# Kernel tuning notes

Measured on AMD Instinct MI355X. Metric: run time of the kernel, lower is better.

The kernel has to match this reference:

```python
import jax, jax.numpy as jnp
import numpy as np

VOCAB = 32000
DIM = 512
B = 1
T = 2048
RANK = 64
TOPK = 16
SLOTS = (256, 64, 16)
INTERVALS = (1, 4, 16)
WIN = 64
PLAYERS = 2
LN_EPS = 1e-5
STD = 0.02


def setup_inputs() -> dict:
    key = jax.random.key(0)
    ks = jax.random.split(key, 12)
    return {
        "input_ids": jax.random.randint(ks[0], (B, T), 0, VOCAB),
        "E": jax.random.normal(ks[1], (VOCAB, DIM), jnp.float32) * STD,
        "Ur": jax.random.normal(ks[2], (3, DIM, RANK), jnp.float32) * STD,
        "Vr": jax.random.normal(ks[3], (3, DIM, RANK), jnp.float32) * STD,
        "m0_0": jax.random.normal(ks[4], (B, SLOTS[0], DIM), jnp.float32) * STD,
        "m0_1": jax.random.normal(ks[5], (B, SLOTS[1], DIM), jnp.float32) * STD,
        "m0_2": jax.random.normal(ks[6], (B, SLOTS[2], DIM), jnp.float32) * STD,
        "Wproj": jax.random.normal(ks[7], (DIM, DIM), jnp.float32) * STD,
        "Wq": jax.random.normal(ks[8], (PLAYERS, DIM, RANK), jnp.float32) * STD,
        "Wk": jax.random.normal(ks[9], (PLAYERS, DIM, RANK), jnp.float32) * STD,
        "ln_in_g": jnp.ones((DIM,), jnp.float32),
        "ln_in_b": jnp.zeros((DIM,), jnp.float32),
        "ln_pred_g": jnp.ones((PLAYERS, DIM), jnp.float32),
        "ln_pred_b": jnp.zeros((PLAYERS, DIM), jnp.float32),
        "ln_out_g": jnp.ones((DIM,), jnp.float32),
        "ln_out_b": jnp.zeros((DIM,), jnp.float32),
    }


def _ln(x, g, b):
    m = jnp.mean(x, axis=-1, keepdims=True)
    v = jnp.mean(jnp.square(x - m), axis=-1, keepdims=True)
    return (x - m) * jax.lax.rsqrt(v + LN_EPS) * g + b


def _memory_scan(s, Ur, Vr, m_init):
    # s: [B, N, D] aligned sequence values; m_init: tuple of [B, S_l, D]
    scale = 1.0 / jnp.sqrt(jnp.float32(RANK))
    x_seq = jnp.swapaxes(s, 0, 1)  # [N, B, D]
    ts = jnp.arange(x_seq.shape[0])
    barange = jnp.arange(s.shape[0])[:, None]

    def step(carry, xs):
        x, t = xs  # x: [B, D]
        read = x
        new_mem = []
        for l, interval in enumerate(INTERVALS):
            M = carry[l]  # [B, S_l, D]
            qr = x @ Ur[l]                                   # [B, r]
            kr = jnp.einsum('bsd,dr->bsr', M, Vr[l])         # [B, S_l, r]
            sc = jnp.einsum('br,bsr->bs', qr, kr) * scale    # low-rank bilinear route
            vals, idx = jax.lax.top_k(sc, TOPK)              # top-k slot routing
            w = jax.nn.softmax(vals, axis=-1)                # [B, K]
            sel = jnp.take_along_axis(M, idx[..., None], axis=1)  # [B, K, D]
            read = read + jnp.einsum('bk,bkd->bd', w, sel)
            gate = jnp.where(t % interval == 0, 1.0, 0.0).astype(x.dtype)
            delta = gate * w[..., None] * x[:, None, :]      # [B, K, D]
            new_mem.append(M.at[barange, idx].add(delta))    # scatter write
        return tuple(new_mem), read

    final_mem, reads = jax.lax.scan(step, m_init, (x_seq, ts))
    return final_mem, jnp.swapaxes(reads, 0, 1)  # [B, N, D]


def reference(input_ids, E, Ur, Vr, m0_0, m0_1, m0_2, Wproj, Wq, Wk,
              ln_in_g, ln_in_b, ln_pred_g, ln_pred_b, ln_out_g, ln_out_b):
    emb = E[input_ids]            # [B, T, D]
    s = emb[:, 1:, :]             # aligned_s = val[:, 1:, :]
    N = s.shape[1]
    scale = 1.0 / jnp.sqrt(jnp.float32(RANK))

    _, q = _memory_scan(s, Ur, Vr, (m0_0, m0_1, m0_2))
    h = _ln(q @ Wproj.T, ln_in_g, ln_in_b)

    offs = jnp.arange(-WIN + 1, 1)
    idx = jnp.arange(N)[:, None] + offs[None, :]   # [N, W]
    valid = idx >= 0
    idxc = jnp.clip(idx, 0, N - 1)

    for p in range(PLAYERS):
        a = jnp.einsum('bnd,dr->bnr', h, Wq[p])
        kf = jnp.einsum('bnd,dr->bnr', h, Wk[p])
        kw = kf[:, idxc]                                       # [B, N, W, r]
        vw = h[:, idxc]                                        # [B, N, W, D]
        sc = jnp.einsum('bnr,bnwr->bnw', a, kw) * scale
        # signed_abs_softmax edge compression
        logits = jnp.where(valid[None], jnp.abs(sc), -1e9)
        w = jax.nn.softmax(logits, axis=-1) * jnp.sign(sc) * valid[None]
        delta = jnp.einsum('bnw,bnwd->bnd', w, vw)
        h = _ln(h + delta, ln_pred_g[p], ln_pred_b[p])         # residual + norm

    out = _ln(h, ln_out_g, ln_out_b)
    return jnp.einsum('bnd,vd->bnv', out, E)  # tied embedding head
```

## Files before the change

### kernel.cpp

```cpp
#include <hip/hip_runtime.h>

#define N_SEQ 2047
#define DIM   512
#define RANK  64
#define VOCAB 32000
#define SCALE 0.125f
#define LN_EPS 1e-5f

typedef __attribute__((ext_vector_type(4))) float  floatx4;
typedef __attribute__((ext_vector_type(8))) __bf16 bf16x8;
typedef __attribute__((ext_vector_type(4))) unsigned short ushortx4;

__device__ __forceinline__ unsigned short f2bf(float x) {
    unsigned int u = __builtin_bit_cast(unsigned int, x);
    return (unsigned short)((u + 0x7fffu + ((u >> 16) & 1u)) >> 16);
}

__device__ __forceinline__ float wave_sum64(float x) {
    int xi;
    xi = __builtin_amdgcn_update_dpp(0, __float_as_int(x), 0x111, 0xf, 0xf, false); x += __int_as_float(xi);
    xi = __builtin_amdgcn_update_dpp(0, __float_as_int(x), 0x112, 0xf, 0xf, false); x += __int_as_float(xi);
    xi = __builtin_amdgcn_update_dpp(0, __float_as_int(x), 0x114, 0xf, 0xf, false); x += __int_as_float(xi);
    xi = __builtin_amdgcn_update_dpp(0, __float_as_int(x), 0x118, 0xf, 0xf, false); x += __int_as_float(xi);
    xi = __builtin_amdgcn_update_dpp(0, __float_as_int(x), 0x142, 0xa, 0xf, false); x += __int_as_float(xi);
    xi = __builtin_amdgcn_update_dpp(0, __float_as_int(x), 0x143, 0x8, 0xf, false); x += __int_as_float(xi);
    return __int_as_float(__builtin_amdgcn_readlane(__float_as_int(x), 63));
}

__global__ __launch_bounds__(128) void k_embed(const int* __restrict__ ids,
                                               const float* __restrict__ E,
                                               float* __restrict__ s,
                                               float* __restrict__ q) {
    int n = blockIdx.x;
    int id = ids[n + 1];
    float4 v = ((const float4*)(E + (size_t)id * DIM))[threadIdx.x];
    ((float4*)(s + (size_t)n * DIM))[threadIdx.x] = v;
    ((float4*)(q + (size_t)n * DIM))[threadIdx.x] = v;
}

__global__ __launch_bounds__(384) void k_proj(const float* __restrict__ s,
                                              const float* __restrict__ Ur,
                                              const float* __restrict__ Vr,
                                              float* __restrict__ qr,
                                              float* __restrict__ xv) {
    __shared__ float s8[8 * DIM];
    int t0 = blockIdx.x * 8;
    for (int i = threadIdx.x; i < 8 * DIM; i += 384) {
        int t = t0 + (i >> 9);
        s8[i] = (t < N_SEQ) ? s[(size_t)t * DIM + (i & 511)] : 0.f;
    }
    __syncthreads();
    int c = threadIdx.x;
    int l = (c % 192) / 64;
    int r = c & 63;
    const float* W = ((c < 192) ? Ur : Vr) + (size_t)l * DIM * RANK + r;
    float acc[8] = {};
    for (int d = 0; d < DIM; d++) {
        float w = W[(size_t)d * RANK];
        #pragma unroll
        for (int i = 0; i < 8; i++) acc[i] += s8[i * DIM + d] * w;
    }
    float* out = ((c < 192) ? qr : xv) + (size_t)l * N_SEQ * RANK;
    #pragma unroll
    for (int i = 0; i < 8; i++) {
        int t = t0 + i;
        if (t < N_SEQ) out[(size_t)t * RANK + r] = acc[i];
    }
}

__global__ __launch_bounds__(64) void k_kr0(const float* __restrict__ m0,
                                            const float* __restrict__ m1,
                                            const float* __restrict__ m2,
                                            const float* __restrict__ Vr,
                                            float* __restrict__ kr) {
    __shared__ float mrow[DIM];
    int sl = blockIdx.x;
    int lvl = (sl < 256) ? 0 : (sl < 320 ? 1 : 2);
    const float* src = (lvl == 0) ? m0 + (size_t)sl * DIM
                     : (lvl == 1) ? m1 + (size_t)(sl - 256) * DIM
                                  : m2 + (size_t)(sl - 320) * DIM;
    for (int i = threadIdx.x; i < DIM / 4; i += 64)
        ((float4*)mrow)[i] = ((const float4*)src)[i];
    __syncthreads();
    const float* W = Vr + (size_t)lvl * DIM * RANK + threadIdx.x;
    float acc = 0.f;
    for (int d = 0; d < DIM; d++) acc += mrow[d] * W[(size_t)d * RANK];
    kr[(size_t)sl * RANK + threadIdx.x] = acc;
}

#define SELECT_BODY(T, QC, QN) { \
    const int t_  = (T); \
    const int tt_ = t_ & 63; \
    const int buf_ = (t_ >> 6) & 1; \
    const int tstage_ = (t_ & ~63) + 64 + tt_; \
    if (tstage_ < N_SEQ) { \
        const float a_ = qrl[(size_t)tstage_ * RANK + lane]; \
        const float c_ = xvl[(size_t)tstage_ * RANK + lane]; \
        qs[(((buf_ ^ 1) << 6) + tt_) * 64 + lane] = a_; \
        xs[(((buf_ ^ 1) << 6) + tt_) * 64 + lane] = c_; \
    } \
    float acc_[G]; \
    _Pragma("unroll") for (int g = 0; g < G; ++g) acc_[g] = 0.f; \
    _Pragma("unroll") for (int rq = 0; rq < 16; ++rq) { \
        const float4 qf_ = QC[rq]; \
        _Pragma("unroll") for (int g = 0; g < G; ++g) { \
            acc_[g] += qf_.x * krr[g][rq * 4 + 0]; \
            acc_[g] += qf_.y * krr[g][rq * 4 + 1]; \
            acc_[g] += qf_.z * krr[g][rq * 4 + 2]; \
            acc_[g] += qf_.w * krr[g][rq * 4 + 3]; \
        } \
    } \
    { const int tn_ = t_ + 1; \
      const int off_ = ((((tn_ >> 6) & 1) << 6) + (tn_ & 63)) * 64; \
      _Pragma("unroll") for (int rq = 0; rq < 16; ++rq) QN[rq] = ((const float4*)(qs + off_))[rq]; } \
    float scf_[G]; unsigned key_[G]; \
    _Pragma("unroll") for (int g = 0; g < G; ++g) { \
        scf_[g] = acc_[g] * SCALE; \
        const unsigned b_ = __float_as_uint(scf_[g]); \
        const unsigned u_ = (b_ & 0x80000000u) ? ~b_ : (b_ | 0x80000000u); \
        key_[g] = ((g << 6) + lane < S) ? u_ : 0u; \
    } \
    unsigned thr_ = 0u; \
    _Pragma("unroll") for (int bit = 31; bit >= 0; --bit) { \
        const unsigned cand_ = thr_ | (1u << bit); \
        int cnt_ = 0; \
        _Pragma("unroll") for (int g = 0; g < G; ++g) cnt_ += (int)__popcll(__ballot(key_[g] >= cand_)); \
        if (cnt_ >= 16) thr_ = cand_; \
    } \
    unsigned long long beq_[G]; unsigned long long bsel_[G]; bool selq_[G]; \
    int cntgt_ = 0; \
    _Pragma("unroll") for (int g = 0; g < G; ++g) { \
        cntgt_ += (int)__popcll(__ballot(key_[g] > thr_)); \
        beq_[g] = __ballot(key_[g] == thr_); \
    } \
    const int needeq_ = 16 - cntgt_; \
    int eqpre_ = 0; \
    _Pragma("unroll") for (int g = 0; g < G; ++g) { \
        const bool isgt_ = key_[g] > thr_; \
        const bool iseq_ = key_[g] == thr_; \
        const int eqrank_ = eqpre_ + (int)__popcll(beq_[g] & ltmask); \
        selq_[g] = isgt_ || (iseq_ && (eqrank_ < needeq_)); \
        bsel_[g] = __ballot(selq_[g]); \
        eqpre_ += (int)__popcll(beq_[g]); \
    } \
    const unsigned tb_ = (thr_ & 0x80000000u) ? (thr_ & 0x7fffffffu) : ~thr_; \
    const float Tf_ = __uint_as_float(tb_); \
    float e_[G]; float es_ = 0.f; \
    _Pragma("unroll") for (int g = 0; g < G; ++g) { \
        e_[g] = selq_[g] ? expf(scf_[g] - Tf_) : 0.f; \
        es_ += e_[g]; \
    } \
    const float inv_ = 1.f / wave_sum64(es_); \
    int pb_ = 0; \
    _Pragma("unroll") for (int g = 0; g < G; ++g) { \
        if (selq_[g]) { \
            const int pos_ = pb_ + (int)__popcll(bsel_[g] & ltmask); \
            float2 o_; o_.x = e_[g] * inv_; o_.y = __int_as_float((g << 6) + lane); \
            selo[(size_t)t_ * 16 + pos_] = o_; \
        } \
        pb_ += (int)__popcll(bsel_[g]); \
    } \
    if ((t_ & IMASK) == 0) { \
        const float* xrow_ = xs + (((size_t)buf_ << 6) + tt_) * 64; \
        _Pragma("unroll") for (int rq = 0; rq < 16; ++rq) { \
            const float4 xf_ = ((const float4*)xrow_)[rq]; \
            _Pragma("unroll") for (int g = 0; g < G; ++g) { \
                const float wg_ = e_[g] * inv_; \
                krr[g][rq * 4 + 0] += wg_ * xf_.x; \
                krr[g][rq * 4 + 1] += wg_ * xf_.y; \
                krr[g][rq * 4 + 2] += wg_ * xf_.z; \
                krr[g][rq * 4 + 3] += wg_ * xf_.w; \
            } \
        } \
    } \
}

template<int S, int IMASK>
__device__ __forceinline__ void select_impl(float* qs, float* xs,
                                            const float* __restrict__ qrl,
                                            const float* __restrict__ xvl,
                                            const float* __restrict__ krl,
                                            float2* __restrict__ selo) {
    constexpr int G = (S + 63) / 64;
    const int lane = threadIdx.x;
    const unsigned long long ltmask = (1ULL << lane) - 1ULL;

    float krr[G][RANK];
    #pragma unroll
    for (int g = 0; g < G; ++g) {
        const int slot = (g << 6) + lane;
        if (slot < S) {
            #pragma unroll
            for (int rq = 0; rq < 16; ++rq) {
                float4 v = ((const float4*)(krl + (size_t)slot * RANK))[rq];
                krr[g][rq * 4 + 0] = v.x; krr[g][rq * 4 + 1] = v.y;
                krr[g][rq * 4 + 2] = v.z; krr[g][rq * 4 + 3] = v.w;
            }
        } else {
            #pragma unroll
            for (int r = 0; r < RANK; ++r) krr[g][r] = 0.f;
        }
    }

    for (int i = 0; i < 64; ++i) {
        qs[i * 64 + lane] = qrl[(size_t)i * RANK + lane];
        xs[i * 64 + lane] = xvl[(size_t)i * RANK + lane];
    }
    __syncthreads();

    float4 qvA[16], qvB[16];
    #pragma unroll
    for (int rq = 0; rq < 16; ++rq) qvA[rq] = ((const float4*)qs)[rq];

    int t = 0;
    for (; t + 1 < N_SEQ; t += 2) {
        SELECT_BODY(t,     qvA, qvB);
        SELECT_BODY(t + 1, qvB, qvA);
    }
    SELECT_BODY(t, qvA, qvB);
}

__global__ __launch_bounds__(64, 1) void k_select_all(const float* __restrict__ qr,
                                                      const float* __restrict__ xv,
                                                      const float* __restrict__ kr0,
                                                      float2* __restrict__ sel) {
    __shared__ float qs[2 * 64 * 64];
    __shared__ float xs[2 * 64 * 64];
    const int l = blockIdx.x;
    if (l == 0)
        select_impl<256, 0>(qs, xs, qr, xv, kr0, sel);
    else if (l == 1)
        select_impl<64, 3>(qs, xs, qr + (size_t)N_SEQ * RANK, xv + (size_t)N_SEQ * RANK,
                           kr0 + 256 * RANK, sel + (size_t)N_SEQ * 16);
    else
        select_impl<16, 15>(qs, xs, qr + (size_t)2 * N_SEQ * RANK, xv + (size_t)2 * N_SEQ * RANK,
                            kr0 + 320 * RANK, sel + (size_t)2 * N_SEQ * 16);
}

template<int S, int IMASK>
__device__ __forceinline__ void apply_impl(float* Ml,
                                           const float* __restrict__ sA,
                                           const float2* __restrict__ selo,
                                           const float* __restrict__ Msrc,
                                           float* __restrict__ q, int chunk) {
    const int lane = threadIdx.x;
    const int c0 = chunk * 64;
    for (int sl = 0; sl < S; ++sl)
        Ml[sl * 64 + lane] = Msrc[(size_t)sl * DIM + c0 + lane];
    __syncthreads();

    float4 svc[8];
    #pragma unroll
    for (int k = 0; k < 8; ++k) svc[k] = ((const float4*)selo)[k];
    float scc = sA[c0 + lane];

    for (int t = 0; t < N_SEQ; ++t) {
        float4 svn[8]; float scn;
        const int tn = (t + 1 < N_SEQ) ? t + 1 : t;
        #pragma unroll
        for (int k = 0; k < 8; ++k) svn[k] = ((const float4*)(selo + (size_t)tn * 16))[k];
        scn = sA[(size_t)tn * DIM + c0 + lane];

        const bool gate = (t & IMASK) == 0;
        float acc = 0.f;
        #pragma unroll
        for (int k = 0; k < 8; ++k) {
            const float w0 = svc[k].x; const int i0 = __float_as_int(svc[k].y);
            const float w1 = svc[k].z; const int i1 = __float_as_int(svc[k].w);
            const float m0v = Ml[i0 * 64 + lane];
            const float m1v = Ml[i1 * 64 + lane];
            acc += w0 * m0v;
            acc += w1 * m1v;
            if (gate) {
                Ml[i0 * 64 + lane] = m0v + w0 * scc;
                Ml[i1 * 64 + lane] = m1v + w1 * scc;
            }
        }
        atomicAdd(&q[(size_t)t * DIM + c0 + lane], acc);
        #pragma unroll
        for (int k = 0; k < 8; ++k) svc[k] = svn[k];
        scc = scn;
    }
}

__global__ __launch_bounds__(64) void k_apply_all(const float* __restrict__ s,
                                                  const float2* __restrict__ sel,
                                                  const float* __restrict__ m0,
                                                  const float* __restrict__ m1,
                                                  const float* __restrict__ m2,
                                                  float* __restrict__ q) {
    __shared__ float Ml[256 * 64];
    const int b = blockIdx.x;
    if (b < 8)
        apply_impl<256, 0>(Ml, s, sel, m0, q, b);
    else if (b < 16)
        apply_impl<64, 3>(Ml, s, sel + (size_t)N_SEQ * 16, m1, q, b - 8);
    else
        apply_impl<16, 15>(Ml, s, sel + (size_t)2 * N_SEQ * 16, m2, q, b - 16);
}

__global__ __launch_bounds__(256) void k_wproj_ln(const float* __restrict__ q,
                                                  const float* __restrict__ Wp,
                                                  const float* __restrict__ g,
                                                  const float* __restrict__ b,
                                                  float* __restrict__ h) {
    __shared__ float q8[8 * DIM];
    __shared__ float hp[8 * DIM];
    int t0 = blockIdx.x * 8;
    for (int i = threadIdx.x; i < 8 * DIM; i += 256) {
        int t = t0 + (i >> 9);
        q8[i] = (t < N_SEQ) ? q[(size_t)t * DIM + (i & 511)] : 0.f;
    }
    __syncthreads();
    int c0 = threadIdx.x * 2;
    float acc0[8] = {}, acc1[8] = {};
    const float* w0 = Wp + (size_t)c0 * DIM;
    const float* w1 = w0 + DIM;
    for (int d = 0; d < DIM; d++) {
        float a0 = w0[d], a1 = w1[d];
        #pragma unroll
        for (int i = 0; i < 8; i++) {
            float qv = q8[i * DIM + d];
            acc0[i] += qv * a0;
            acc1[i] += qv * a1;
        }
    }
    #pragma unroll
    for (int i = 0; i < 8; i++) {
        hp[i * DIM + c0]     = acc0[i];
        hp[i * DIM + c0 + 1] = acc1[i];
    }
    __syncthreads();
    int rowi = threadIdx.x >> 5;
    int l32  = threadIdx.x & 31;
    int t = t0 + rowi;
    if (t < N_SEQ) {
        float sum = 0.f, sq = 0.f;
        #pragma unroll
        for (int u = 0; u < 16; u++) {
            float x = hp[rowi * DIM + l32 + u * 32];
            sum += x; sq += x * x;
        }
        #pragma unroll
        for (int off = 16; off >= 1; off >>= 1) {
            sum += __shfl_xor(sum, off, 32);
            sq  += __shfl_xor(sq,  off, 32);
        }
        float mean = sum * (1.f / DIM);
        float var  = sq * (1.f / DIM) - mean * mean;
        float inv  = rsqrtf(var + LN_EPS);
        #pragma unroll
        for (int u = 0; u < 16; u++) {
            int d = l32 + u * 32;
            float x = hp[rowi * DIM + d];
            h[(size_t)t * DIM + d] = (x - mean) * inv * g[d] + b[d];
        }
    }
}

__global__ __launch_bounds__(128) void k_qk(const float* __restrict__ h,
                                            const float* __restrict__ Wq,
                                            const float* __restrict__ Wk,
                                            float* __restrict__ a,
                                            float* __restrict__ kf) {
    __shared__ float h8[8 * DIM];
    int t0 = blockIdx.x * 8;
    for (int i = threadIdx.x; i < 8 * DIM; i += 128) {
        int t = t0 + (i >> 9);
        h8[i] = (t < N_SEQ) ? h[(size_t)t * DIM + (i & 511)] : 0.f;
    }
    __syncthreads();
    int c = threadIdx.x;
    int r = c & 63;
    const float* W = ((c < 64) ? Wq : Wk) + r;
    float acc[8] = {};
    for (int d = 0; d < DIM; d++) {
        float w = W[(size_t)d * RANK];
        #pragma unroll
        for (int i = 0; i < 8; i++) acc[i] += h8[i * DIM + d] * w;
    }
    float* out = (c < 64) ? a : kf;
    #pragma unroll
    for (int i = 0; i < 8; i++) {
        int t = t0 + i;
        if (t < N_SEQ) out[(size_t)t * RANK + r] = acc[i];
    }
}

__global__ __launch_bounds__(64) void k_attn(const float* __restrict__ hin,
                                             const float* __restrict__ a,
                                             const float* __restrict__ kf,
                                             const float* __restrict__ g,
                                             const float* __restrict__ b,
                                             float* __restrict__ hout) {
    __shared__ float a_s[64];
    __shared__ float w_s[64];
    int t = blockIdx.x;
    int lane = threadIdx.x;
    a_s[lane] = a[(size_t)t * RANK + lane];
    __syncthreads();
    int src  = t - 63 + lane;
    int srcc = src < 0 ? 0 : src;
    const float* kr_ = kf + (size_t)srcc * RANK;
    float sc = 0.f;
    #pragma unroll 8
    for (int r = 0; r < RANK; r++) sc += a_s[r] * kr_[r];
    sc *= SCALE;
    float logit = (src >= 0) ? fabsf(sc) : -1e9f;
    float m = logit;
    #pragma unroll
    for (int off = 32; off >= 1; off >>= 1) m = fmaxf(m, __shfl_xor(m, off, 64));
    float e = expf(logit - m);
    float sum = e;
    #pragma unroll
    for (int off = 32; off >= 1; off >>= 1) sum += __shfl_xor(sum, off, 64);
    float sgn = (sc > 0.f) ? 1.f : ((sc < 0.f) ? -1.f : 0.f);
    float w = (src >= 0) ? (e / sum) * sgn : 0.f;
    w_s[lane] = w;
    __syncthreads();
    float acc[8] = {};
    int basej = t - 63;
    for (int j = 0; j < 64; j++) {
        float wj = w_s[j];
        int sj = basej + j; sj = sj < 0 ? 0 : sj;
        const float* hr = hin + (size_t)sj * DIM + lane;
        #pragma unroll
        for (int u = 0; u < 8; u++) acc[u] += wj * hr[u * 64];
    }
    const float* hrow = hin + (size_t)t * DIM + lane;
    float x[8]; float sum2 = 0.f, sq = 0.f;
    #pragma unroll
    for (int u = 0; u < 8; u++) {
        x[u] = hrow[u * 64] + acc[u];
        sum2 += x[u]; sq += x[u] * x[u];
    }
    #pragma unroll
    for (int off = 32; off >= 1; off >>= 1) {
        sum2 += __shfl_xor(sum2, off, 64);
        sq   += __shfl_xor(sq,   off, 64);
    }
    float mean = sum2 * (1.f / DIM);
    float var  = sq * (1.f / DIM) - mean * mean;
    float inv  = rsqrtf(var + LN_EPS);
    #pragma unroll
    for (int u = 0; u < 8; u++) {
        int d = lane + u * 64;
        hout[(size_t)t * DIM + d] = (x[u] - mean) * inv * g[d] + b[d];
    }
}

__global__ __launch_bounds__(64) void k_ln_out(const float* __restrict__ hin,
                                               const float* __restrict__ g,
                                               const float* __restrict__ b,
                                               float* __restrict__ hP) {
    int t = blockIdx.x;
    int lane = threadIdx.x;
    if (t >= N_SEQ) {
        #pragma unroll
        for (int u = 0; u < 8; u++) hP[(size_t)t * DIM + lane + u * 64] = 0.f;
        return;
    }
    const float* hrow = hin + (size_t)t * DIM + lane;
    float x[8]; float sum = 0.f, sq = 0.f;
    #pragma unroll
    for (int u = 0; u < 8; u++) {
        x[u] = hrow[u * 64];
        sum += x[u]; sq += x[u] * x[u];
    }
    #pragma unroll
    for (int off = 32; off >= 1; off >>= 1) {
        sum += __shfl_xor(sum, off, 64);
        sq  += __shfl_xor(sq,  off, 64);
    }
    float mean = sum * (1.f / DIM);
    float var  = sq * (1.f / DIM) - mean * mean;
    float inv  = rsqrtf(var + LN_EPS);
    #pragma unroll
    for (int u = 0; u < 8; u++) {
        int d = lane + u * 64;
        hP[(size_t)t * DIM + d] = (x[u] - mean) * inv * g[d] + b[d];
    }
}

__global__ __launch_bounds__(256) void k_gemm(const float* __restrict__ A,
                                              const float* __restrict__ E,
                                              float* __restrict__ C) {
    __shared__ unsigned short As[128 * 64];
    __shared__ unsigned short Bs[128 * 64];
    int bm = blockIdx.y, bn = blockIdx.x;
    int tid = threadIdx.x;
    int lane = tid & 63, wave = tid >> 6;
    int wm = (wave >> 1) << 6, wn = (wave & 1) << 6;
    floatx4 acc[4][4] = {};
    for (int k0 = 0; k0 < DIM; k0 += 64) {
        #pragma unroll
        for (int ch = 0; ch < 8; ch++) {
            int f4 = ch * 256 + tid;
            int el = f4 * 4;
            int row = el >> 6;
            int kk = el & 63;
            int csw = (kk >> 3) ^ (row & 7);
            int dst = row * 64 + csw * 8 + (kk & 7);
            float4 av = *(const float4*)(A + (size_t)(bm * 128 + row) * DIM + k0 + kk);
            ushortx4 ua = { f2bf(av.x), f2bf(av.y), f2bf(av.z), f2bf(av.w) };
            *(ushortx4*)&As[dst] = ua;
            float4 bv = *(const float4*)(E + (size_t)(bn * 128 + row) * DIM + k0 + kk);
            ushortx4 ub = { f2bf(bv.x), f2bf(bv.y), f2bf(bv.z), f2bf(bv.w) };
            *(ushortx4*)&Bs[dst] = ub;
        }
        __syncthreads();
        int mr = lane & 15, qd = lane >> 4;
        #pragma unroll
        for (int kh = 0; kh < 2; kh++) {
            bf16x8 af[4], bfr[4];
            #pragma unroll
            for (int i = 0; i < 4; i++) {
                int row = wm + i * 16 + mr;
                int c = kh * 4 + qd;
                af[i] = *(const bf16x8*)&As[row * 64 + ((c ^ (row & 7)) << 3)];
            }
            #pragma unroll
            for (int j = 0; j < 4; j++) {
                int row = wn + j * 16 + mr;
                int c = kh * 4 + qd;
                bfr[j] = *(const bf16x8*)&Bs[row * 64 + ((c ^ (row & 7)) << 3)];
            }
            #pragma unroll
            for (int i = 0; i < 4; i++)
                #pragma unroll
                for (int j = 0; j < 4; j++)
                    acc[i][j] = __builtin_amdgcn_mfma_f32_16x16x32_bf16(af[i], bfr[j], acc[i][j], 0, 0, 0);
        }
        __syncthreads();
    }
    int lr = lane >> 4, lc = lane & 15;
    #pragma unroll
    for (int i = 0; i < 4; i++)
        #pragma unroll
        for (int j = 0; j < 4; j++)
            #pragma unroll
            for (int reg = 0; reg < 4; reg++) {
                int gr = bm * 128 + wm + i * 16 + lr * 4 + reg;
                int gc = bn * 128 + wn + j * 16 + lc;
                if (gr < N_SEQ) C[(size_t)gr * VOCAB + gc] = acc[i][j][reg];
            }
}

extern "C" void kernel_launch(void* const* d_in, const int* in_sizes, int n_in,
                              void* d_out, int out_size, void* d_ws, size_t ws_size,
                              hipStream_t stream) {
    (void)in_sizes; (void)n_in; (void)out_size; (void)ws_size;
    const int*   ids  = (const int*)d_in[0];
    const float* E    = (const float*)d_in[1];
    const float* Ur   = (const float*)d_in[2];
    const float* Vr   = (const float*)d_in[3];
    const float* m0   = (const float*)d_in[4];
    const float* m1   = (const float*)d_in[5];
    const float* m2   = (const float*)d_in[6];
    const float* Wp   = (const float*)d_in[7];
    const float* Wq   = (const float*)d_in[8];
    const float* Wk   = (const float*)d_in[9];
    const float* lig  = (const float*)d_in[10];
    const float* lib  = (const float*)d_in[11];
    const float* lpg  = (const float*)d_in[12];
    const float* lpb  = (const float*)d_in[13];
    const float* log_ = (const float*)d_in[14];
    const float* lob  = (const float*)d_in[15];
    float* out = (float*)d_out;

    float* ws = (float*)d_ws;
    size_t off = 0;
    auto alloc = [&](size_t n) { float* p = ws + off; off += (n + 255) & ~(size_t)255; return p; };
    float* s   = alloc((size_t)N_SEQ * DIM);
    float* q   = alloc((size_t)N_SEQ * DIM);
    float* qr  = alloc((size_t)3 * N_SEQ * RANK);
    float* xv  = alloc((size_t)3 * N_SEQ * RANK);
    float* kr  = alloc((size_t)336 * RANK);
    float* sel = alloc((size_t)3 * N_SEQ * 16 * 2);
    float* hA  = alloc((size_t)N_SEQ * DIM);
    float* hB  = alloc((size_t)N_SEQ * DIM);
    float* ab  = alloc((size_t)N_SEQ * RANK);
    float* kfb = alloc((size_t)N_SEQ * RANK);
    float* hP  = alloc((size_t)2048 * DIM);

    k_embed     <<<N_SEQ, 128, 0, stream>>>(ids, E, s, q);
    k_proj      <<<256, 384, 0, stream>>>(s, Ur, Vr, qr, xv);
    k_kr0       <<<336, 64, 0, stream>>>(m0, m1, m2, Vr, kr);
    k_select_all<<<3, 64, 0, stream>>>(qr, xv, kr, (float2*)sel);
    k_apply_all <<<24, 64, 0, stream>>>(s, (const float2*)sel, m0, m1, m2, q);
    k_wproj_ln  <<<256, 256, 0, stream>>>(q, Wp, lig, lib, hA);
    k_qk        <<<256, 128, 0, stream>>>(hA, Wq, Wk, ab, kfb);
    k_attn      <<<N_SEQ, 64, 0, stream>>>(hA, ab, kfb, lpg, lpb, hB);
    k_qk        <<<256, 128, 0, stream>>>(hB, Wq + DIM * RANK, Wk + DIM * RANK, ab, kfb);
    k_attn      <<<N_SEQ, 64, 0, stream>>>(hB, ab, kfb, lpg + DIM, lpb + DIM, hA);
    k_ln_out    <<<2048, 64, 0, stream>>>(hA, log_, lob, hP);
    dim3 gg(VOCAB / 128, 2048 / 128);
    k_gemm      <<<gg, 256, 0, stream>>>(hP, E, out);
}
```

Measured before the change: 10.69 ms.

## Split sequential top-k select into a selector wave and score-computing worker waves

The serial memory-routing select kernel moves from one 64-thread wave per level to 320 threads. Wave 0 performs the top-k threshold search, now resolving two bits per step, and writes the selected weights to shared memory. The other waves each own one slot's key vector, apply the previous step's rank-1 update and compute the next step's score one step ahead. A diagonal correction term is added so the lookahead score matches the updated key. This shortens the per-token critical path, at the cost of two block barriers per timestep and extra shared-memory traffic.

New measurement: 9.122 ms. 1.17x faster.

```diff
diff --git a/kernel.cpp b/kernel.cpp
--- a/kernel.cpp
+++ b/kernel.cpp
@@ -88,152 +88,204 @@
     kr[(size_t)sl * RANK + threadIdx.x] = acc;
 }
 
-#define SELECT_BODY(T, QC, QN) { \
-    const int t_  = (T); \
-    const int tt_ = t_ & 63; \
-    const int buf_ = (t_ >> 6) & 1; \
-    const int tstage_ = (t_ & ~63) + 64 + tt_; \
-    if (tstage_ < N_SEQ) { \
-        const float a_ = qrl[(size_t)tstage_ * RANK + lane]; \
-        const float c_ = xvl[(size_t)tstage_ * RANK + lane]; \
-        qs[(((buf_ ^ 1) << 6) + tt_) * 64 + lane] = a_; \
-        xs[(((buf_ ^ 1) << 6) + tt_) * 64 + lane] = c_; \
-    } \
-    float acc_[G]; \
-    _Pragma("unroll") for (int g = 0; g < G; ++g) acc_[g] = 0.f; \
-    _Pragma("unroll") for (int rq = 0; rq < 16; ++rq) { \
-        const float4 qf_ = QC[rq]; \
-        _Pragma("unroll") for (int g = 0; g < G; ++g) { \
-            acc_[g] += qf_.x * krr[g][rq * 4 + 0]; \
-            acc_[g] += qf_.y * krr[g][rq * 4 + 1]; \
-            acc_[g] += qf_.z * krr[g][rq * 4 + 2]; \
-            acc_[g] += qf_.w * krr[g][rq * 4 + 3]; \
-        } \
-    } \
-    { const int tn_ = t_ + 1; \
-      const int off_ = ((((tn_ >> 6) & 1) << 6) + (tn_ & 63)) * 64; \
-      _Pragma("unroll") for (int rq = 0; rq < 16; ++rq) QN[rq] = ((const float4*)(qs + off_))[rq]; } \
-    float scf_[G]; unsigned key_[G]; \
-    _Pragma("unroll") for (int g = 0; g < G; ++g) { \
-        scf_[g] = acc_[g] * SCALE; \
-        const unsigned b_ = __float_as_uint(scf_[g]); \
-        const unsigned u_ = (b_ & 0x80000000u) ? ~b_ : (b_ | 0x80000000u); \
-        key_[g] = ((g << 6) + lane < S) ? u_ : 0u; \
-    } \
-    unsigned thr_ = 0u; \
-    _Pragma("unroll") for (int bit = 31; bit >= 0; --bit) { \
-        const unsigned cand_ = thr_ | (1u << bit); \
-        int cnt_ = 0; \
-        _Pragma("unroll") for (int g = 0; g < G; ++g) cnt_ += (int)__popcll(__ballot(key_[g] >= cand_)); \
-        if (cnt_ >= 16) thr_ = cand_; \
-    } \
-    unsigned long long beq_[G]; unsigned long long bsel_[G]; bool selq_[G]; \
-    int cntgt_ = 0; \
-    _Pragma("unroll") for (int g = 0; g < G; ++g) { \
-        cntgt_ += (int)__popcll(__ballot(key_[g] > thr_)); \
-        beq_[g] = __ballot(key_[g] == thr_); \
-    } \
-    const int needeq_ = 16 - cntgt_; \
-    int eqpre_ = 0; \
-    _Pragma("unroll") for (int g = 0; g < G; ++g) { \
-        const bool isgt_ = key_[g] > thr_; \
-        const bool iseq_ = key_[g] == thr_; \
-        const int eqrank_ = eqpre_ + (int)__popcll(beq_[g] & ltmask); \
-        selq_[g] = isgt_ || (iseq_ && (eqrank_ < needeq_)); \
-        bsel_[g] = __ballot(selq_[g]); \
-        eqpre_ += (int)__popcll(beq_[g]); \
-    } \
-    const unsigned tb_ = (thr_ & 0x80000000u) ? (thr_ & 0x7fffffffu) : ~thr_; \
-    const float Tf_ = __uint_as_float(tb_); \
-    float e_[G]; float es_ = 0.f; \
-    _Pragma("unroll") for (int g = 0; g < G; ++g) { \
-        e_[g] = selq_[g] ? expf(scf_[g] - Tf_) : 0.f; \
-        es_ += e_[g]; \
-    } \
-    const float inv_ = 1.f / wave_sum64(es_); \
-    int pb_ = 0; \
-    _Pragma("unroll") for (int g = 0; g < G; ++g) { \
-        if (selq_[g]) { \
-            const int pos_ = pb_ + (int)__popcll(bsel_[g] & ltmask); \
-            float2 o_; o_.x = e_[g] * inv_; o_.y = __int_as_float((g << 6) + lane); \
-            selo[(size_t)t_ * 16 + pos_] = o_; \
-        } \
-        pb_ += (int)__popcll(bsel_[g]); \
-    } \
-    if ((t_ & IMASK) == 0) { \
-        const float* xrow_ = xs + (((size_t)buf_ << 6) + tt_) * 64; \
-        _Pragma("unroll") for (int rq = 0; rq < 16; ++rq) { \
-            const float4 xf_ = ((const float4*)xrow_)[rq]; \
-            _Pragma("unroll") for (int g = 0; g < G; ++g) { \
-                const float wg_ = e_[g] * inv_; \
-                krr[g][rq * 4 + 0] += wg_ * xf_.x; \
-                krr[g][rq * 4 + 1] += wg_ * xf_.y; \
-                krr[g][rq * 4 + 2] += wg_ * xf_.z; \
-                krr[g][rq * 4 + 3] += wg_ * xf_.w; \
-            } \
-        } \
-    } \
-}
-
 template<int S, int IMASK>
-__device__ __forceinline__ void select_impl(float* qs, float* xs,
+__device__ __forceinline__ void select_impl(float (*qs)[32][64], float (*xs)[32][64],
+                                            float* scs, float* wsel_s, int* isel_s,
                                             const float* __restrict__ qrl,
                                             const float* __restrict__ xvl,
                                             const float* __restrict__ krl,
                                             float2* __restrict__ selo) {
     constexpr int G = (S + 63) / 64;
-    const int lane = threadIdx.x;
+    const int tid  = threadIdx.x;
+    const int wave = tid >> 6;
+    const int lane = tid & 63;
     const unsigned long long ltmask = (1ULL << lane) - 1ULL;
 
-    float krr[G][RANK];
-    #pragma unroll
-    for (int g = 0; g < G; ++g) {
-        const int slot = (g << 6) + lane;
-        if (slot < S) {
-            #pragma unroll
-            for (int rq = 0; rq < 16; ++rq) {
-                float4 v = ((const float4*)(krl + (size_t)slot * RANK))[rq];
-                krr[g][rq * 4 + 0] = v.x; krr[g][rq * 4 + 1] = v.y;
-                krr[g][rq * 4 + 2] = v.z; krr[g][rq * 4 + 3] = v.w;
+    for (int row = wave; row < 32; row += 5) {
+        qs[0][row][lane] = qrl[(size_t)row * RANK + lane];
+        xs[0][row][lane] = xvl[(size_t)row * RANK + lane];
+    }
+    if (tid < 256) scs[tid] = -3.0e38f;
+
+    const int  slot     = (wave >= 1) ? (((wave - 1) << 6) + lane) : -1;
+    const bool isWorker = (wave >= 1) && (slot < S);
+
+    float krr[RANK];
+    if (isWorker) {
+        #pragma unroll
+        for (int i = 0; i < 16; ++i)
+            ((floatx4*)krr)[i] = ((const floatx4*)(krl + (size_t)slot * RANK))[i];
+    } else {
+        #pragma unroll
+        for (int r = 0; r < RANK; ++r) krr[r] = 0.f;
+    }
+
+    float qstage = 0.f, xstage = 0.f;
+    if (wave == 1) qstage = qrl[(size_t)32 * RANK + lane];
+    if (wave == 2) xstage = xvl[(size_t)32 * RANK + lane];
+
+    __syncthreads();
+
+    if (isWorker) {
+        float acc = 0.f;
+        #pragma unroll
+        for (int i = 0; i < 16; ++i) {
+            float4 qf = ((const float4*)qs[0][0])[i];
+            acc += qf.x * krr[i*4+0] + qf.y * krr[i*4+1] + qf.z * krr[i*4+2] + qf.w * krr[i*4+3];
+        }
+        scs[slot] = acc * SCALE;
+    }
+    float wprev = 0.f;
+    __syncthreads();
+
+    for (int t = 0; t < N_SEQ; ++t) {
+        const int gate = ((t & IMASK) == 0);
+        float sc_raw = 0.f, dgl = 0.f;
+
+        if (wave == 0) {
+            float scf[G]; unsigned key[G];
+            #pragma unroll
+            for (int g = 0; g < G; ++g) {
+                float v = scs[(g << 6) + lane];
+                scf[g] = v;
+                unsigned bb = __float_as_uint(v);
+                key[g] = (bb & 0x80000000u) ? ~bb : (bb | 0x80000000u);
+            }
+            unsigned thr = 0u;
+            #pragma unroll
+            for (int bit = 30; bit >= 0; bit -= 2) {
+                const unsigned cLo = thr | (1u << bit);
+                const unsigned cHi = thr | (2u << bit);
+                const unsigned cBo = thr | (3u << bit);
+                int nLo = 0, nHi = 0, nBo = 0;
+                #pragma unroll
+                for (int g = 0; g < G; ++g) {
+                    nLo += (int)__popcll(__ballot(key[g] >= cLo));
+                    nHi += (int)__popcll(__ballot(key[g] >= cHi));
+                    nBo += (int)__popcll(__ballot(key[g] >= cBo));
+                }
+                if (nHi >= 16)      thr = (nBo >= 16) ? cBo : cHi;
+                else if (nLo >= 16) thr = cLo;
+            }
+            unsigned long long beq[G], bsel[G]; bool selq[G];
+            int cntgt = 0;
+            #pragma unroll
+            for (int g = 0; g < G; ++g) {
+                cntgt += (int)__popcll(__ballot(key[g] > thr));
+                beq[g] = __ballot(key[g] == thr);
+            }
+            const int needeq = 16 - cntgt;
+            int eqpre = 0;
+            #pragma unroll
+            for (int g = 0; g < G; ++g) {
+                const bool isgt = key[g] > thr;
+                const bool iseq = key[g] == thr;
+                const int eqrank = eqpre + (int)__popcll(beq[g] & ltmask);
+                selq[g] = isgt || (iseq && (eqrank < needeq));
+                bsel[g] = __ballot(selq[g]);
+                eqpre += (int)__popcll(beq[g]);
+            }
+            const unsigned tb = (thr & 0x80000000u) ? (thr & 0x7fffffffu) : ~thr;
+            const float Tf = __uint_as_float(tb);
+            float e[G]; float es = 0.f;
+            #pragma unroll
+            for (int g = 0; g < G; ++g) {
+                e[g] = selq[g] ? expf(scf[g] - Tf) : 0.f;
+                es += e[g];
+            }
+            const float inv = 1.f / wave_sum64(es);
+            int pb = 0;
+            #pragma unroll
+            for (int g = 0; g < G; ++g) {
+                if (selq[g]) {
+                    const int pos = pb + (int)__popcll(bsel[g] & ltmask);
+                    const float w = e[g] * inv;
+                    const int sl = (g << 6) + lane;
+                    float2 o; o.x = w; o.y = __int_as_float(sl);
+                    selo[(size_t)t * 16 + pos] = o;
+                    wsel_s[pos] = w;
+                    isel_s[pos] = sl;
+                }
+                pb += (int)__popcll(bsel[g]);
             }
         } else {
-            #pragma unroll
-            for (int r = 0; r < RANK; ++r) krr[g][r] = 0.f;
-        }
-    }
-
-    for (int i = 0; i < 64; ++i) {
-        qs[i * 64 + lane] = qrl[(size_t)i * RANK + lane];
-        xs[i * 64 + lane] = xvl[(size_t)i * RANK + lane];
-    }
-    __syncthreads();
-
-    float4 qvA[16], qvB[16];
-    #pragma unroll
-    for (int rq = 0; rq < 16; ++rq) qvA[rq] = ((const float4*)qs)[rq];
-
-    int t = 0;
-    for (; t + 1 < N_SEQ; t += 2) {
-        SELECT_BODY(t,     qvA, qvB);
-        SELECT_BODY(t + 1, qvB, qvA);
-    }
-    SELECT_BODY(t, qvA, qvB);
-}
-
-__global__ __launch_bounds__(64, 1) void k_select_all(const float* __restrict__ qr,
-                                                      const float* __restrict__ xv,
-                                                      const float* __restrict__ kr0,
-                                                      float2* __restrict__ sel) {
-    __shared__ float qs[2 * 64 * 64];
-    __shared__ float xs[2 * 64 * 64];
+            const int tp = (t > 0) ? t - 1 : 0;
+            const int tn = t + 1;
+            const int tq = (tn < N_SEQ) ? tn : t;
+            const float* xrow_p = xs[(tp >> 5) & 1][tp & 31];
+            const float* qrow_n = qs[(tq >> 5) & 1][tq & 31];
+            const float* xrow_t = xs[(t  >> 5) & 1][t  & 31];
+            if (isWorker) {
+                #pragma unroll
+                for (int i = 0; i < 16; ++i) {
+                    float4 xf = ((const float4*)xrow_p)[i];
+                    krr[i*4+0] += wprev * xf.x; krr[i*4+1] += wprev * xf.y;
+                    krr[i*4+2] += wprev * xf.z; krr[i*4+3] += wprev * xf.w;
+                }
+                float acc = 0.f;
+                #pragma unroll
+                for (int i = 0; i < 16; ++i) {
+                    float4 qf = ((const float4*)qrow_n)[i];
+                    acc += qf.x * krr[i*4+0] + qf.y * krr[i*4+1]
+                         + qf.z * krr[i*4+2] + qf.w * krr[i*4+3];
+                }
+                sc_raw = acc;
+            }
+            dgl = wave_sum64(qrow_n[lane] * xrow_t[lane]);
+            if (wave == 1) {
+                const int uw = t + 32;
+                if (uw < N_SEQ) qs[(uw >> 5) & 1][uw & 31][lane] = qstage;
+                const int ul = t + 33;
+                if (ul < N_SEQ) qstage = qrl[(size_t)ul * RANK + lane];
+            }
+            if (wave == 2) {
+                const int uw = t + 32;
+                if (uw < N_SEQ) xs[(uw >> 5) & 1][uw & 31][lane] = xstage;
+                const int ul = t + 33;
+                if (ul < N_SEQ) xstage = xvl[(size_t)ul * RANK + lane];
+            }
+        }
+        __syncthreads();
+        if (wave != 0) {
+            float wloc = 0.f;
+            if (isWorker) {
+                #pragma unroll
+                for (int j = 0; j < 4; ++j) {
+                    int4   ii = ((const int4*)isel_s)[j];
+                    float4 ww = ((const float4*)wsel_s)[j];
+                    wloc = (ii.x == slot) ? ww.x : wloc;
+                    wloc = (ii.y == slot) ? ww.y : wloc;
+                    wloc = (ii.z == slot) ? ww.z : wloc;
+                    wloc = (ii.w == slot) ? ww.w : wloc;
+                }
+                const float corr = gate ? wloc * dgl : 0.f;
+                scs[slot] = (sc_raw + corr) * SCALE;
+            }
+            wprev = gate ? wloc : 0.f;
+        }
+        __syncthreads();
+    }
+}
+
+__global__ __launch_bounds__(320, 1) void k_select_all(const float* __restrict__ qr,
+                                                       const float* __restrict__ xv,
+                                                       const float* __restrict__ kr0,
+                                                       float2* __restrict__ sel) {
+    __shared__ float qs[2][32][64];
+    __shared__ float xs[2][32][64];
+    __shared__ float scs[256];
+    __shared__ float wsel_s[16];
+    __shared__ int   isel_s[16];
     const int l = blockIdx.x;
     if (l == 0)
-        select_impl<256, 0>(qs, xs, qr, xv, kr0, sel);
+        select_impl<256, 0>(qs, xs, scs, wsel_s, isel_s, qr, xv, kr0, sel);
     else if (l == 1)
-        select_impl<64, 3>(qs, xs, qr + (size_t)N_SEQ * RANK, xv + (size_t)N_SEQ * RANK,
+        select_impl<64, 3>(qs, xs, scs, wsel_s, isel_s,
+                           qr + (size_t)N_SEQ * RANK, xv + (size_t)N_SEQ * RANK,
                            kr0 + 256 * RANK, sel + (size_t)N_SEQ * 16);
     else
-        select_impl<16, 15>(qs, xs, qr + (size_t)2 * N_SEQ * RANK, xv + (size_t)2 * N_SEQ * RANK,
+        select_impl<16, 15>(qs, xs, scs, wsel_s, isel_s,
+                            qr + (size_t)2 * N_SEQ * RANK, xv + (size_t)2 * N_SEQ * RANK,
                             kr0 + 320 * RANK, sel + (size_t)2 * N_SEQ * 16);
 }
 
@@ -586,7 +638,7 @@
     k_embed     <<<N_SEQ, 128, 0, stream>>>(ids, E, s, q);
     k_proj      <<<256, 384, 0, stream>>>(s, Ur, Vr, qr, xv);
     k_kr0       <<<336, 64, 0, stream>>>(m0, m1, m2, Vr, kr);
-    k_select_all<<<3, 64, 0, stream>>>(qr, xv, kr, (float2*)sel);
+    k_select_all<<<3, 320, 0, stream>>>(qr, xv, kr, (float2*)sel);
     k_apply_all <<<24, 64, 0, stream>>>(s, (const float2*)sel, m0, m1, m2, q);
     k_wproj_ln  <<<256, 256, 0, stream>>>(q, Wp, lig, lib, hA);
     k_qk        <<<256, 128, 0, stream>>>(hA, Wq, Wk, ab, kfb);
```
